# Kernel tuning notes

Measured on AMD Instinct MI355X. Metric: run time of the kernel, lower is better.

Reference implementation:

```python
import jax, jax.numpy as jnp
import numpy as np

MAX_DISP = 4  # max_displacement == pad_size; kernel_size == 1, stride == 1


def setup_inputs() -> dict:
    key = jax.random.key(0)
    k1, k2 = jax.random.split(key)
    B, C, H, W = 8, 256, 96, 128
    in1 = jax.random.normal(k1, (B, C, H, W), dtype=jnp.float32)
    in2 = jax.random.normal(k2, (B, C, H, W), dtype=jnp.float32)
    return {"in1": in1, "in2": in2}


def reference(in1, in2):
    # Local cost-volume correlation: for each pixel (h,w) and each displacement
    # (dy,dx) in [-4,4]^2, mean over channels of in1[...,h,w] * in2[...,h+dy,w+dx]
    # with zero padding outside the image. Output: [B, 81, H, W].
    B, C, H, W = in1.shape
    d = MAX_DISP
    p2 = jnp.pad(in2, ((0, 0), (0, 0), (d, d), (d, d)))
    outs = []
    # fixed 9x9 displacement set (structural, not a data-dim loop)
    for dy in range(2 * d + 1):
        for dx in range(2 * d + 1):
            shifted = jax.lax.dynamic_slice(p2, (0, 0, dy, dx), (B, C, H, W))
            outs.append(jnp.mean(in1 * shifted, axis=1))  # [B, H, W]
    return jnp.stack(outs, axis=1)  # [B, 81, H, W]
```

## Files before the change

### kernel.cpp

```cpp
#include <hip/hip_runtime.h>


#define CH 256
#define HALFC 128
#define HH 96
#define WW 128
#define CS (HH * WW)

__device__ __forceinline__ float wshr1(float x) {
  union { float f; int i; } u, o;
  u.f = x;
  o.i = __builtin_amdgcn_update_dpp(0, u.i, 0x138, 0xF, 0xF, true);
  return o.f;
}
__device__ __forceinline__ float wshl1(float x) {
  union { float f; int i; } u, o;
  u.f = x;
  o.i = __builtin_amdgcn_update_dpp(0, u.i, 0x130, 0xF, 0xF, true);
  return o.f;
}

__global__ __launch_bounds__(512, 4) void corr_split(
    const float* __restrict__ in1, const float* __restrict__ in2,
    float* __restrict__ out)
{
  const int j    = blockIdx.x;
  const int xcd  = j & 7;
  const int s    = j >> 3;
  const int dy   = s % 9;
  const int tq   = s / 9;
  const int tile = tq * 8 + xcd;
  const int band = tile % 12;
  const int b    = tile / 12;
  const int dyo  = dy - 4;

  const int tid  = threadIdx.x;
  const int half = tid >> 8;
  const int t    = tid & 255;
  const int wv   = t >> 6;
  const int lane = t & 63;
  const int r    = lane >> 5;
  const int g    = lane & 31;
  const int h    = band * 8 + wv * 2 + r;
  const int px   = g << 2;
  const int r2   = h + dyo;
  const bool rowok = (unsigned)r2 < (unsigned)HH;
  const int r2c  = r2 < 0 ? 0 : (r2 > HH - 1 ? HH - 1 : r2);

  const float* __restrict__ p1 =
      in1 + (((size_t)b * CH + half * HALFC) * HH + h)   * WW + px;
  const float* __restrict__ p2 =
      in2 + (((size_t)b * CH + half * HALFC) * HH + r2c) * WW + px;

  float acc[4][9];
#pragma unroll
  for (int p = 0; p < 4; ++p)
#pragma unroll
    for (int d = 0; d < 9; ++d) acc[p][d] = 0.f;

#pragma unroll 2
  for (int c = 0; c < HALFC; ++c) {
    float4 a4 = *(const float4*)p1;  p1 += CS;
    float4 m4 = *(const float4*)p2;  p2 += CS;

    float w[12];
    w[0] = wshr1(m4.x); w[1] = wshr1(m4.y); w[2] = wshr1(m4.z); w[3] = wshr1(m4.w);
    w[4] = m4.x; w[5] = m4.y; w[6] = m4.z; w[7] = m4.w;
    w[8] = wshl1(m4.x); w[9] = wshl1(m4.y); w[10] = wshl1(m4.z); w[11] = wshl1(m4.w);

    const float av[4] = {a4.x, a4.y, a4.z, a4.w};
#pragma unroll
    for (int p = 0; p < 4; ++p)
#pragma unroll
      for (int d = 0; d < 9; ++d)
        acc[p][d] = fmaf(av[p], w[p + d], acc[p][d]);
  }

  __shared__ float red[256][11];
#pragma unroll
  for (int pp = 0; pp < 4; ++pp) {
    if (half) {
#pragma unroll
      for (int d = 0; d < 9; ++d) red[t][d] = acc[pp][d];
    }
    __syncthreads();
    if (!half) {
#pragma unroll
      for (int d = 0; d < 9; ++d) acc[pp][d] += red[t][d];
    }
    __syncthreads();
  }

  if (!half) {
    const float sc = 1.0f / (float)CH;
    float* po = out + (((size_t)b * 81 + dy * 9) * HH + h) * WW + px;
#pragma unroll
    for (int d = 0; d < 9; ++d) {
      float v[4];
#pragma unroll
      for (int p = 0; p < 4; ++p) {
        const int col2 = px + p + d - 4;
        const bool ok  = rowok && ((unsigned)col2 < (unsigned)WW);
        v[p] = ok ? acc[p][d] * sc : 0.f;
      }
      *(float4*)po = make_float4(v[0], v[1], v[2], v[3]);
      po += (size_t)CS;
    }
  }
}

extern "C" void kernel_launch(void* const* d_in, const int* in_sizes, int n_in,
                              void* d_out, int out_size, void* d_ws, size_t ws_size,
                              hipStream_t stream) {
  const float* in1 = (const float*)d_in[0];
  const float* in2 = (const float*)d_in[1];
  float* out = (float*)d_out;
  hipLaunchKernelGGL(corr_split, dim3(864), dim3(512), 0, stream, in1, in2, out);
}
```

Baseline: 299.9 us.

## Compute three dy displacements per block to reuse in1 loads across rows

Each block now handles three vertical displacements at once, with each thread covering 2 pixels instead of 4 and a whole 64-lane wave covering one full row. The in1 value loaded per channel is reused for three in2 rows, which cuts redundant in1 traffic and reduces the grid from 864 to 576 blocks. Because each wave now spans 128 columns with 2 pixels per lane, horizontal neighbours come from chained DPP lane shifts (two hops for the ±2..4 offsets). The costs are more accumulator registers (54 instead of 36), a larger shared reduction buffer, and fewer blocks.

```diff
diff --git a/kernel.cpp b/kernel.cpp
--- a/kernel.cpp
+++ b/kernel.cpp
@@ -20,91 +20,112 @@
   return o.f;
 }
 
-__global__ __launch_bounds__(512, 4) void corr_split(
+__device__ __forceinline__ void row_fma(float (&ak)[2][9], const float2 a,
+                                        const float2 m) {
+  float w[10];
+  w[2] = wshr1(m.x);  w[3] = wshr1(m.y);
+  w[0] = wshr1(w[2]); w[1] = wshr1(w[3]);
+  w[4] = m.x;         w[5] = m.y;
+  w[6] = wshl1(m.x);  w[7] = wshl1(m.y);
+  w[8] = wshl1(w[6]); w[9] = wshl1(w[7]);
+#pragma unroll
+  for (int d = 0; d < 9; ++d) {
+    ak[0][d] = fmaf(a.x, w[d],     ak[0][d]);
+    ak[1][d] = fmaf(a.y, w[d + 1], ak[1][d]);
+  }
+}
+
+__global__ __launch_bounds__(512, 4) void corr3dy(
     const float* __restrict__ in1, const float* __restrict__ in2,
     float* __restrict__ out)
 {
   const int j    = blockIdx.x;
   const int xcd  = j & 7;
   const int s    = j >> 3;
-  const int dy   = s % 9;
-  const int tq   = s / 9;
+  const int dyg  = s % 3;
+  const int tq   = s / 3;
   const int tile = tq * 8 + xcd;
-  const int band = tile % 12;
-  const int b    = tile / 12;
-  const int dyo  = dy - 4;
+  const int band = tile % 24;
+  const int b    = tile / 24;
+  const int D    = dyg * 3 - 4;
 
   const int tid  = threadIdx.x;
   const int half = tid >> 8;
   const int t    = tid & 255;
-  const int wv   = t >> 6;
+  const int wr   = t >> 6;
   const int lane = t & 63;
-  const int r    = lane >> 5;
-  const int g    = lane & 31;
-  const int h    = band * 8 + wv * 2 + r;
-  const int px   = g << 2;
-  const int r2   = h + dyo;
-  const bool rowok = (unsigned)r2 < (unsigned)HH;
-  const int r2c  = r2 < 0 ? 0 : (r2 > HH - 1 ? HH - 1 : r2);
+  const int h    = band * 4 + wr;
+  const int px   = lane << 1;
 
-  const float* __restrict__ p1 =
-      in1 + (((size_t)b * CH + half * HALFC) * HH + h)   * WW + px;
-  const float* __restrict__ p2 =
-      in2 + (((size_t)b * CH + half * HALFC) * HH + r2c) * WW + px;
+  bool rowok[3];
+  int  r2c[3];
+#pragma unroll
+  for (int k = 0; k < 3; ++k) {
+    const int r2 = h + D + k;
+    rowok[k] = (unsigned)r2 < (unsigned)HH;
+    r2c[k]   = r2 < 0 ? 0 : (r2 > HH - 1 ? HH - 1 : r2);
+  }
 
-  float acc[4][9];
+  const size_t cbase = ((size_t)b * CH + half * HALFC) * HH;
+  const float* __restrict__ p1  = in1 + (cbase + h)      * WW + px;
+  const float* __restrict__ p20 = in2 + (cbase + r2c[0]) * WW + px;
+  const float* __restrict__ p21 = in2 + (cbase + r2c[1]) * WW + px;
+  const float* __restrict__ p22 = in2 + (cbase + r2c[2]) * WW + px;
+
+  float acc[3][2][9];
 #pragma unroll
-  for (int p = 0; p < 4; ++p)
+  for (int k = 0; k < 3; ++k)
 #pragma unroll
-    for (int d = 0; d < 9; ++d) acc[p][d] = 0.f;
+    for (int p = 0; p < 2; ++p)
+#pragma unroll
+      for (int d = 0; d < 9; ++d) acc[k][p][d] = 0.f;
 
 #pragma unroll 2
   for (int c = 0; c < HALFC; ++c) {
-    float4 a4 = *(const float4*)p1;  p1 += CS;
-    float4 m4 = *(const float4*)p2;  p2 += CS;
-
-    float w[12];
-    w[0] = wshr1(m4.x); w[1] = wshr1(m4.y); w[2] = wshr1(m4.z); w[3] = wshr1(m4.w);
-    w[4] = m4.x; w[5] = m4.y; w[6] = m4.z; w[7] = m4.w;
-    w[8] = wshl1(m4.x); w[9] = wshl1(m4.y); w[10] = wshl1(m4.z); w[11] = wshl1(m4.w);
-
-    const float av[4] = {a4.x, a4.y, a4.z, a4.w};
-#pragma unroll
-    for (int p = 0; p < 4; ++p)
-#pragma unroll
-      for (int d = 0; d < 9; ++d)
-        acc[p][d] = fmaf(av[p], w[p + d], acc[p][d]);
+    const float2 a  = *(const float2*)p1;   p1  += CS;
+    const float2 m0 = *(const float2*)p20;  p20 += CS;
+    const float2 m1 = *(const float2*)p21;  p21 += CS;
+    const float2 m2 = *(const float2*)p22;  p22 += CS;
+    row_fma(acc[0], a, m0);
+    row_fma(acc[1], a, m1);
+    row_fma(acc[2], a, m2);
   }
 
-  __shared__ float red[256][11];
+  __shared__ float red[256][19];
 #pragma unroll
-  for (int pp = 0; pp < 4; ++pp) {
+  for (int k = 0; k < 3; ++k) {
     if (half) {
 #pragma unroll
-      for (int d = 0; d < 9; ++d) red[t][d] = acc[pp][d];
+      for (int p = 0; p < 2; ++p)
+#pragma unroll
+        for (int d = 0; d < 9; ++d) red[t][p * 9 + d] = acc[k][p][d];
     }
     __syncthreads();
     if (!half) {
 #pragma unroll
-      for (int d = 0; d < 9; ++d) acc[pp][d] += red[t][d];
+      for (int p = 0; p < 2; ++p)
+#pragma unroll
+        for (int d = 0; d < 9; ++d) acc[k][p][d] += red[t][p * 9 + d];
     }
     __syncthreads();
   }
 
   if (!half) {
     const float sc = 1.0f / (float)CH;
-    float* po = out + (((size_t)b * 81 + dy * 9) * HH + h) * WW + px;
 #pragma unroll
-    for (int d = 0; d < 9; ++d) {
-      float v[4];
+    for (int k = 0; k < 3; ++k) {
+      const int dy = dyg * 3 + k;
+      float* po = out + (((size_t)b * 81 + dy * 9) * HH + h) * WW + px;
 #pragma unroll
-      for (int p = 0; p < 4; ++p) {
-        const int col2 = px + p + d - 4;
-        const bool ok  = rowok && ((unsigned)col2 < (unsigned)WW);
-        v[p] = ok ? acc[p][d] * sc : 0.f;
+      for (int d = 0; d < 9; ++d) {
+        float2 v;
+        const int c0 = px + d - 4;
+        const int c1 = px + 1 + d - 4;
+        v.x = (rowok[k] && (unsigned)c0 < (unsigned)WW) ? acc[k][0][d] * sc : 0.f;
+        v.y = (rowok[k] && (unsigned)c1 < (unsigned)WW) ? acc[k][1][d] * sc : 0.f;
+        *(float2*)po = v;
+        po += (size_t)CS;
       }
-      *(float4*)po = make_float4(v[0], v[1], v[2], v[3]);
-      po += (size_t)CS;
     }
   }
 }
@@ -115,5 +136,5 @@
   const float* in1 = (const float*)d_in[0];
   const float* in2 = (const float*)d_in[1];
   float* out = (float*)d_out;
-  hipLaunchKernelGGL(corr_split, dim3(864), dim3(512), 0, stream, in1, in2, out);
+  hipLaunchKernelGGL(corr3dy, dim3(576), dim3(512), 0, stream, in1, in2, out);
 }
```

After: 337.3 us. 1.12x slower.
